# Performance work log

Measured on AMD Instinct MI355X. Metric: run time of the kernel, lower is better.

Reference implementation:

```python
import jax, jax.numpy as jnp
import numpy as np

HEADS = 16
LN_EPS = 1e-6

def _layernorm(x, scale, bias):
    mu = jnp.mean(x, axis=-1, keepdims=True)
    var = jnp.mean(jnp.square(x - mu), axis=-1, keepdims=True)
    return (x - mu) * jax.lax.rsqrt(var + LN_EPS) * scale + bias

def setup_inputs() -> dict:
    key = jax.random.key(0)
    ks = jax.random.split(key, 5)
    B, L, D, F = 2, 2048, 1024, 4096
    s = lambda fan_in: 1.0 / np.sqrt(fan_in)
    return {
        'x': jax.random.normal(ks[0], (B, L, D), jnp.float32),
        'ln1_scale': jnp.ones((D,), jnp.float32),
        'ln1_bias': jnp.zeros((D,), jnp.float32),
        'w_qkv': jax.random.normal(ks[1], (D, 3 * D), jnp.float32) * s(D),
        'w_proj': jax.random.normal(ks[2], (D, D), jnp.float32) * s(D),
        'b_proj': jnp.zeros((D,), jnp.float32),
        'ln2_scale': jnp.ones((D,), jnp.float32),
        'ln2_bias': jnp.zeros((D,), jnp.float32),
        'w_mlp1': jax.random.normal(ks[3], (D, F), jnp.float32) * s(D),
        'b_mlp1': jnp.zeros((F,), jnp.float32),
        'w_mlp2': jax.random.normal(ks[4], (F, D), jnp.float32) * s(F),
        'b_mlp2': jnp.zeros((D,), jnp.float32),
    }

def reference(x, ln1_scale, ln1_bias, w_qkv, w_proj, b_proj,
              ln2_scale, ln2_bias, w_mlp1, b_mlp1, w_mlp2, b_mlp2):
    B, L, D = x.shape
    H = HEADS
    hd = D // H
    # pre-norm attention
    h = _layernorm(x, ln1_scale, ln1_bias)
    qkv = h @ w_qkv  # [B,L,3D]
    q, k, v = jnp.split(qkv, 3, axis=-1)
    q = q.reshape(B, L, H, hd).transpose(0, 2, 1, 3)  # [B,H,L,hd]
    k = k.reshape(B, L, H, hd).transpose(0, 2, 1, 3)
    v = v.reshape(B, L, H, hd).transpose(0, 2, 1, 3)
    scale = jnp.sqrt(jnp.float32(hd))
    scores = jnp.einsum('bhqd,bhkd->bhqk', q, k) / scale  # [B,H,L,L]
    attn = jax.nn.softmax(scores, axis=-1)
    out = jnp.einsum('bhqk,bhkd->bhqd', attn, v)  # [B,H,L,hd]
    out = out.transpose(0, 2, 1, 3).reshape(B, L, D)
    x = x + out @ w_proj + b_proj
    # pre-norm MLP
    h = _layernorm(x, ln2_scale, ln2_bias)
    m = jax.nn.gelu(h @ w_mlp1 + b_mlp1, approximate=True)
    return x + m @ w_mlp2 + b_mlp2
```

## Files before the change

### kernel.cpp

```cpp
#include <hip/hip_runtime.h>
#include <hip/hip_bf16.h>
#include <cstdint>
#include <cstddef>

typedef __bf16 bf16;
typedef __bf16 bf16x8 __attribute__((ext_vector_type(8)));
typedef float f32x4 __attribute__((ext_vector_type(4)));
typedef short short4v __attribute__((ext_vector_type(4)));
typedef unsigned uint2v __attribute__((ext_vector_type(2)));

#define GLB_AS(p) ((const __attribute__((address_space(1))) unsigned*)(unsigned long long)(p))
#define LDS_AS(p) ((__attribute__((address_space(3))) unsigned*)(unsigned)(unsigned long long)(p))

__device__ __forceinline__ void g2l16(const void* g, void* l) {
  __builtin_amdgcn_global_load_lds(GLB_AS(g), LDS_AS(l), 16, 0, 0);
}

__device__ __forceinline__ short f2bf(float x) {
  bf16 h = (bf16)x;
  return __builtin_bit_cast(short, h);
}

__device__ __forceinline__ unsigned pk_bf16(float a, float b) {
  __hip_bfloat162 h = __float22bfloat162_rn(float2{a, b});
  unsigned u;
  __builtin_memcpy(&u, &h, 4);
  return u;
}

extern "C" __device__ __attribute__((const)) float __ocml_native_exp2_f32(float);
extern "C" __device__ __attribute__((const)) float __ocml_native_recip_f32(float);
__device__ __forceinline__ float fast_exp2(float x) {
  return __ocml_native_exp2_f32(x);
}
__device__ __forceinline__ float fast_tanh(float a) {
  float e = __ocml_native_exp2_f32(a * 2.8853900817779268f);
  return 1.f - 2.f * __ocml_native_recip_f32(e + 1.f);
}

constexpr int MROWS = 4096;
constexpr size_t ATILE = (size_t)MROWS * 32;

#define QSCALE 0.18033688011112042f

__device__ __forceinline__ void transpose_body(
    const float* __restrict__ in, bf16* __restrict__ out, int K, int N,
    int bx, int by, float (*tile)[33], int tid)
{
  int tx = tid & 31, ty = tid >> 5;
  int n0 = bx * 32, k0 = by * 32;
  for (int i = ty; i < 32; i += 8)
    tile[i][tx] = in[(size_t)(k0 + i) * N + n0 + tx];
  __syncthreads();
  bf16* obase = out + (size_t)(k0 >> 5) * N * 32;
  for (int i = ty; i < 32; i += 8)
    obase[(size_t)(n0 + i) * 32 + tx] = (bf16)tile[tx][i];
}

__device__ __forceinline__ void ln_body(
    const float* __restrict__ x, const float* __restrict__ sc,
    const float* __restrict__ bi, bf16* __restrict__ out,
    int row, float* wsum, float* wsq, int tid)
{
  const float* xr = x + (size_t)row * 1024;
  int c = tid * 4;
  float4 xv = *(const float4*)(xr + c);
  float s = xv.x + xv.y + xv.z + xv.w;
  float q = xv.x * xv.x + xv.y * xv.y + xv.z * xv.z + xv.w * xv.w;
#pragma unroll
  for (int off = 1; off < 64; off <<= 1) {
    s += __shfl_xor(s, off);
    q += __shfl_xor(q, off);
  }
  int wv = tid >> 6;
  if ((tid & 63) == 0) { wsum[wv] = s; wsq[wv] = q; }
  __syncthreads();
  s = wsum[0] + wsum[1] + wsum[2] + wsum[3];
  q = wsq[0] + wsq[1] + wsq[2] + wsq[3];
  float mean = s * (1.f / 1024.f);
  float var = q * (1.f / 1024.f) - mean * mean;
  float rstd = rsqrtf(var + 1e-6f);
  float4 scv = *(const float4*)(sc + c);
  float4 biv = *(const float4*)(bi + c);
  bf16* o = out + (size_t)(c >> 5) * ATILE + (size_t)row * 32 + (c & 31);
  o[0] = (bf16)((xv.x - mean) * rstd * scv.x + biv.x);
  o[1] = (bf16)((xv.y - mean) * rstd * scv.y + biv.y);
  o[2] = (bf16)((xv.z - mean) * rstd * scv.z + biv.z);
  o[3] = (bf16)((xv.w - mean) * rstd * scv.w + biv.w);
}

__global__ __launch_bounds__(256) void prep_kernel(
    const float* __restrict__ wqkv, const float* __restrict__ wproj,
    const float* __restrict__ wmlp1, const float* __restrict__ wmlp2,
    bf16* __restrict__ wqkv_t, bf16* __restrict__ wproj_t,
    bf16* __restrict__ wmlp1_t, bf16* __restrict__ wmlp2_t,
    const float* __restrict__ x, const float* __restrict__ ln1s,
    const float* __restrict__ ln1b, bf16* __restrict__ hbuf)
{
  __shared__ float tile[32][33];
  __shared__ float wsum[4], wsq[4];
  int bid = blockIdx.x, tid = threadIdx.x;
  if (bid < 3072)
    transpose_body(wqkv, wqkv_t, 1024, 3072, bid % 96, bid / 96, tile, tid);
  else if (bid < 4096) {
    int i = bid - 3072;
    transpose_body(wproj, wproj_t, 1024, 1024, i % 32, i / 32, tile, tid);
  } else if (bid < 8192) {
    int i = bid - 4096;
    transpose_body(wmlp1, wmlp1_t, 1024, 4096, i % 128, i / 128, tile, tid);
  } else if (bid < 12288) {
    int i = bid - 8192;
    transpose_body(wmlp2, wmlp2_t, 4096, 1024, i % 32, i / 32, tile, tid);
  } else {
    ln_body(x, ln1s, ln1b, hbuf, bid - 12288, wsum, wsq, tid);
  }
}

__global__ __launch_bounds__(256) void ln_kernel(
    const float* __restrict__ x, const float* __restrict__ sc,
    const float* __restrict__ bi, bf16* __restrict__ out)
{
  __shared__ float wsum[4], wsq[4];
  ln_body(x, sc, bi, out, blockIdx.x, wsum, wsq, threadIdx.x);
}

template <int MT, int NT, int KS, int EPI>
__global__ __launch_bounds__(256) void gemm_tt(
    const bf16* __restrict__ A, const bf16* __restrict__ Bt,
    int N, int K,
    const float* __restrict__ bias, const float* __restrict__ resid,
    float* __restrict__ outf, bf16* __restrict__ ob0,
    bf16* __restrict__ ob1, bf16* __restrict__ ob2)
{
  constexpr int TM = MT * 32, TN = NT * 32;
  __shared__ __align__(16) bf16 As[2][TM * 32 * KS];
  __shared__ __align__(16) bf16 Bs[2][TN * 32 * KS];
  const int tid = threadIdx.x, lane = tid & 63, wave = tid >> 6;
  const int wm = wave >> 1, wn = wave & 1;
  const int quad = lane >> 4, l16 = lane & 15;

  int flat = blockIdx.x + gridDim.x * blockIdx.y;
  int xcd = flat & 7, rr = flat >> 3;
  int npx = gridDim.x >> 3;
  int bn = xcd * npx + (rr % npx);
  int bm = rr / npx;

  const size_t astride = ATILE;
  const size_t bstride = (size_t)N * 32;
  const bf16* Abase = A + (size_t)bm * TM * 32 + (size_t)lane * 8;
  const bf16* Bbase = Bt + (size_t)bn * TN * 32 + (size_t)lane * 8;

  f32x4 acc[MT][NT] = {};
  const int KT = K / (32 * KS);

  auto stage = [&](int buf, int kt) {
#pragma unroll
    for (int ks = 0; ks < KS; ks++) {
      const bf16* Ab = Abase + (size_t)(kt * KS + ks) * astride;
      const bf16* Bb = Bbase + (size_t)(kt * KS + ks) * bstride;
#pragma unroll
      for (int i = 0; i < MT / 2; i++)
        g2l16(Ab + (wave + 4 * i) * 512, &As[buf][ks * TM * 32 + (wave + 4 * i) * 512]);
#pragma unroll
      for (int i = 0; i < NT / 2; i++)
        g2l16(Bb + (wave + 4 * i) * 512, &Bs[buf][ks * TN * 32 + (wave + 4 * i) * 512]);
    }
  };

  stage(0, 0);
  int buf = 0;
  for (int kt = 0; kt < KT; kt++) {
    __syncthreads();
    if (kt + 1 < KT) stage(buf ^ 1, kt + 1);
#pragma unroll
    for (int kk = 0; kk < KS; kk++) {
      bf16x8 af[MT], bfr[NT];
#pragma unroll
      for (int mt = 0; mt < MT; mt++)
        af[mt] = *(const bf16x8*)&As[buf][kk * TM * 32 + (wm * MT * 16 + mt * 16 + l16) * 32 + quad * 8];
#pragma unroll
      for (int nt = 0; nt < NT; nt++)
        bfr[nt] = *(const bf16x8*)&Bs[buf][kk * TN * 32 + (wn * NT * 16 + nt * 16 + l16) * 32 + quad * 8];
#pragma unroll
      for (int mt = 0; mt < MT; mt++)
#pragma unroll
        for (int nt = 0; nt < NT; nt++)
          acc[mt][nt] = __builtin_amdgcn_mfma_f32_16x16x32_bf16(af[mt], bfr[nt], acc[mt][nt], 0, 0, 0);
    }
    buf ^= 1;
  }

#pragma unroll
  for (int mt = 0; mt < MT; mt++) {
#pragma unroll
    for (int nt = 0; nt < NT; nt++) {
      int row0 = bm * TM + wm * MT * 16 + mt * 16 + quad * 4;
      int col = bn * TN + wn * NT * 16 + nt * 16 + l16;
      if (EPI == 0) {
        int b = row0 >> 11, l = row0 & 2047;
        int which = col >> 10, d = col & 1023;
        int hh = d >> 6, hdi = d & 63;
        size_t bh = (size_t)(b * 16 + hh);
        if (which == 0) {
#pragma unroll
          for (int r = 0; r < 4; r++)
            ob0[(bh * 2048 + l + r) * 64 + hdi] = (bf16)(acc[mt][nt][r] * QSCALE);
        } else if (which == 1) {
#pragma unroll
          for (int r = 0; r < 4; r++)
            ob1[(bh * 2048 + l + r) * 64 + hdi] = (bf16)acc[mt][nt][r];
        } else {
          short4v v4;
#pragma unroll
          for (int r = 0; r < 4; r++) v4[r] = f2bf(acc[mt][nt][r]);
          *(short4v*)&ob2[(bh * 64 + hdi) * 2048 + l] = v4;
        }
      } else {
#pragma unroll
        for (int r = 0; r < 4; r++) {
          int row = row0 + r;
          float v = acc[mt][nt][r];
          if (EPI == 1) {
            size_t idx = (size_t)row * N + col;
            outf[idx] = v + bias[col] + resid[idx];
          } else {
            float t = v + bias[col];
            float a = 0.7978845608028654f * t * (1.f + 0.044715f * t * t);
            float g = 0.5f * t * (1.f + fast_tanh(a));
            ob0[(size_t)(col >> 5) * ATILE + (size_t)row * 32 + (col & 31)] = (bf16)g;
          }
        }
      }
    }
  }
}

__global__ __launch_bounds__(256, 2) void flash_attn(
    const bf16* __restrict__ Q, const bf16* __restrict__ Kg,
    const bf16* __restrict__ Vg, bf16* __restrict__ O)
{
  __shared__ __align__(16) bf16 Ks[128 * 72];
  __shared__ __align__(16) bf16 Vs[64 * 136];
  const int tid = threadIdx.x, lane = tid & 63, wave = tid >> 6;
  const int quad = lane >> 4, l16 = lane & 15;
  const int qt = blockIdx.x, bh = blockIdx.y;
  const int b = bh >> 4, h = bh & 15;

  const bf16* qg = Q + ((size_t)bh * 2048 + qt * 128) * 64;
  const bf16* kg = Kg + (size_t)bh * 2048 * 64;
  const bf16* vg = Vg + (size_t)bh * 64 * 2048;

  bf16x8 qf[2][2];
#pragma unroll
  for (int s = 0; s < 2; s++)
#pragma unroll
    for (int kk = 0; kk < 2; kk++)
      qf[s][kk] = *(const bf16x8*)&qg[(size_t)(wave * 32 + s * 16 + l16) * 64 + kk * 32 + quad * 8];

  f32x4 oacc[2][4] = {};
  float lrow[2] = {0.f, 0.f};

  bf16x8 kreg[4], vreg[4];
#pragma unroll
  for (int i = 0; i < 4; i++) {
    int t = tid + i * 256;
    kreg[i] = *(const bf16x8*)&kg[(size_t)(t >> 3) * 64 + (t & 7) * 8];
    vreg[i] = *(const bf16x8*)&vg[(size_t)(t >> 4) * 2048 + (t & 15) * 8];
  }

  for (int kt = 0; kt < 16; kt++) {
    __syncthreads();
#pragma unroll
    for (int i = 0; i < 4; i++) {
      int t = tid + i * 256;
      *(bf16x8*)&Ks[(t >> 3) * 72 + (t & 7) * 8] = kreg[i];
      *(bf16x8*)&Vs[(t >> 4) * 136 + (t & 15) * 8] = vreg[i];
    }
    __syncthreads();
    if (kt < 15) {
#pragma unroll
      for (int i = 0; i < 4; i++) {
        int t = tid + i * 256;
        kreg[i] = *(const bf16x8*)&kg[((size_t)(kt + 1) * 128 + (t >> 3)) * 64 + (t & 7) * 8];
        vreg[i] = *(const bf16x8*)&vg[(size_t)(t >> 4) * 2048 + (kt + 1) * 128 + (t & 15) * 8];
      }
    }

    f32x4 sacc[2][8] = {};
#pragma unroll
    for (int kk = 0; kk < 2; kk++) {
#pragma unroll
      for (int ct = 0; ct < 8; ct++) {
        bf16x8 kf = *(const bf16x8*)&Ks[(ct * 16 + l16) * 72 + kk * 32 + quad * 8];
        sacc[0][ct] = __builtin_amdgcn_mfma_f32_16x16x32_bf16(kf, qf[0][kk], sacc[0][ct], 0, 0, 0);
        sacc[1][ct] = __builtin_amdgcn_mfma_f32_16x16x32_bf16(kf, qf[1][kk], sacc[1][ct], 0, 0, 0);
      }
    }

    short4v pf[2][8];
#pragma unroll
    for (int s = 0; s < 2; s++) {
      float sum = 0.f;
#pragma unroll
      for (int ct = 0; ct < 8; ct++) {
        float p0 = fast_exp2(sacc[s][ct][0]);
        float p1 = fast_exp2(sacc[s][ct][1]);
        float p2 = fast_exp2(sacc[s][ct][2]);
        float p3 = fast_exp2(sacc[s][ct][3]);
        sum += (p0 + p1) + (p2 + p3);
        uint2v u;
        u[0] = pk_bf16(p0, p1);
        u[1] = pk_bf16(p2, p3);
        pf[s][ct] = __builtin_bit_cast(short4v, u);
      }
      lrow[s] += sum;
    }

#pragma unroll
    for (int ot = 0; ot < 4; ot++) {
#pragma unroll
      for (int ct = 0; ct < 8; ct++) {
        short4v vf = *(const short4v*)&Vs[(ot * 16 + l16) * 136 + ct * 16 + quad * 4];
        oacc[0][ot] = __builtin_amdgcn_mfma_f32_16x16x16bf16_1k(vf, pf[0][ct], oacc[0][ot], 0, 0, 0);
        oacc[1][ot] = __builtin_amdgcn_mfma_f32_16x16x16bf16_1k(vf, pf[1][ct], oacc[1][ot], 0, 0, 0);
      }
    }
  }

#pragma unroll
  for (int s = 0; s < 2; s++) {
    float l = lrow[s];
    l += __shfl_xor(l, 16);
    l += __shfl_xor(l, 32);
    float inv = 1.f / l;
    int qrow = qt * 128 + wave * 32 + s * 16 + l16;
    size_t grow = (size_t)b * 2048 + qrow;
#pragma unroll
    for (int ot = 0; ot < 4; ot++) {
      int col = h * 64 + ot * 16 + quad * 4;
      short4v o4;
#pragma unroll
      for (int r = 0; r < 4; r++) o4[r] = f2bf(oacc[s][ot][r] * inv);
      *(short4v*)&O[(size_t)(col >> 5) * ATILE + grow * 32 + (col & 31)] = o4;
    }
  }
}

extern "C" void kernel_launch(void* const* d_in, const int* in_sizes, int n_in,
                              void* d_out, int out_size, void* d_ws, size_t ws_size,
                              hipStream_t stream)
{
  const float* x     = (const float*)d_in[0];
  const float* ln1s  = (const float*)d_in[1];
  const float* ln1b  = (const float*)d_in[2];
  const float* wqkv  = (const float*)d_in[3];
  const float* wproj = (const float*)d_in[4];
  const float* bproj = (const float*)d_in[5];
  const float* ln2s  = (const float*)d_in[6];
  const float* ln2b  = (const float*)d_in[7];
  const float* wmlp1 = (const float*)d_in[8];
  const float* bmlp1 = (const float*)d_in[9];
  const float* wmlp2 = (const float*)d_in[10];
  const float* bmlp2 = (const float*)d_in[11];
  float* out = (float*)d_out;

  char* ws = (char*)d_ws;
  bf16* wqkv_t  = (bf16*)(ws + 0);
  bf16* wproj_t = (bf16*)(ws + 6291456);
  bf16* wmlp1_t = (bf16*)(ws + 8388608);
  bf16* wmlp2_t = (bf16*)(ws + 16777216);
  bf16* hbuf    = (bf16*)(ws + 25165824);
  bf16* qb      = (bf16*)(ws + 33554432);
  bf16* kb      = (bf16*)(ws + 41943040);
  bf16* vb      = (bf16*)(ws + 50331648);
  bf16* aout    = (bf16*)(ws + 58720256);
  bf16* mbuf    = (bf16*)(ws + 33554432);

  prep_kernel<<<16384, 256, 0, stream>>>(wqkv, wproj, wmlp1, wmlp2,
                                         wqkv_t, wproj_t, wmlp1_t, wmlp2_t,
                                         x, ln1s, ln1b, hbuf);
  gemm_tt<4, 4, 1, 0><<<dim3(24, 32), 256, 0, stream>>>(hbuf, wqkv_t, 3072, 1024,
                                                        nullptr, nullptr, nullptr, qb, kb, vb);
  flash_attn<<<dim3(16, 32), 256, 0, stream>>>(qb, kb, vb, aout);
  gemm_tt<2, 4, 2, 1><<<dim3(8, 64), 256, 0, stream>>>(aout, wproj_t, 1024, 1024,
                                                       bproj, x, out, nullptr, nullptr, nullptr);
  ln_kernel<<<4096, 256, 0, stream>>>(out, ln2s, ln2b, hbuf);
  gemm_tt<4, 4, 1, 2><<<dim3(32, 32), 256, 0, stream>>>(hbuf, wmlp1_t, 4096, 1024,
                                                        bmlp1, nullptr, nullptr, mbuf, nullptr, nullptr);
  gemm_tt<2, 4, 2, 1><<<dim3(8, 64), 256, 0, stream>>>(mbuf, wmlp2_t, 1024, 4096,
                                                       bmlp2, out, out, nullptr, nullptr, nullptr);
}
```

Baseline: 313.3 us.

## Use 8 waves per attention block with XOR-swizzled LDS and MFMA priority

The flash attention kernel goes from 4 waves each handling 32 query rows to 8 waves each handling 16 rows. This halves per-thread register state and raises the occupancy target. The padded K/V LDS tiles are replaced by unpadded tiles with an XOR swizzle to avoid bank conflicts. s_setprio is raised around the MFMA phases so waves can overlap matrix work with softmax. Each K fragment read from LDS is now reused for only one query subtile instead of two, so LDS read traffic per MFMA increases.

```diff
diff --git a/kernel.cpp b/kernel.cpp
--- a/kernel.cpp
+++ b/kernel.cpp
@@ -235,12 +235,12 @@
   }
 }
 
-__global__ __launch_bounds__(256, 2) void flash_attn(
+__global__ __launch_bounds__(512, 4) void flash_attn(
     const bf16* __restrict__ Q, const bf16* __restrict__ Kg,
     const bf16* __restrict__ Vg, bf16* __restrict__ O)
 {
-  __shared__ __align__(16) bf16 Ks[128 * 72];
-  __shared__ __align__(16) bf16 Vs[64 * 136];
+  __shared__ __align__(16) bf16 Ks[128 * 64];
+  __shared__ __align__(16) bf16 Vs[64 * 128];
   const int tid = threadIdx.x, lane = tid & 63, wave = tid >> 6;
   const int quad = lane >> 4, l16 = lane & 15;
   const int qt = blockIdx.x, bh = blockIdx.y;
@@ -250,20 +250,21 @@
   const bf16* kg = Kg + (size_t)bh * 2048 * 64;
   const bf16* vg = Vg + (size_t)bh * 64 * 2048;
 
-  bf16x8 qf[2][2];
-#pragma unroll
-  for (int s = 0; s < 2; s++)
-#pragma unroll
-    for (int kk = 0; kk < 2; kk++)
-      qf[s][kk] = *(const bf16x8*)&qg[(size_t)(wave * 32 + s * 16 + l16) * 64 + kk * 32 + quad * 8];
-
-  f32x4 oacc[2][4] = {};
-  float lrow[2] = {0.f, 0.f};
-
-  bf16x8 kreg[4], vreg[4];
-#pragma unroll
-  for (int i = 0; i < 4; i++) {
-    int t = tid + i * 256;
+  const int kw0 = ((tid >> 3) << 7) + (((tid & 7) << 4) ^ (((tid >> 3) & 7) << 4));
+  const int vw0 = ((tid >> 4) << 8) + (((tid & 15) << 4) ^ (((tid >> 4) & 7) << 4));
+
+  bf16x8 qf[2];
+#pragma unroll
+  for (int kk = 0; kk < 2; kk++)
+    qf[kk] = *(const bf16x8*)&qg[(size_t)(wave * 16 + l16) * 64 + kk * 32 + quad * 8];
+
+  f32x4 oacc[4] = {};
+  float lrow = 0.f;
+
+  bf16x8 kreg[2], vreg[2];
+#pragma unroll
+  for (int i = 0; i < 2; i++) {
+    int t = tid + i * 512;
     kreg[i] = *(const bf16x8*)&kg[(size_t)(t >> 3) * 64 + (t & 7) * 8];
     vreg[i] = *(const bf16x8*)&vg[(size_t)(t >> 4) * 2048 + (t & 15) * 8];
   }
@@ -271,76 +272,79 @@
   for (int kt = 0; kt < 16; kt++) {
     __syncthreads();
 #pragma unroll
-    for (int i = 0; i < 4; i++) {
-      int t = tid + i * 256;
-      *(bf16x8*)&Ks[(t >> 3) * 72 + (t & 7) * 8] = kreg[i];
-      *(bf16x8*)&Vs[(t >> 4) * 136 + (t & 15) * 8] = vreg[i];
+    for (int i = 0; i < 2; i++) {
+      *(bf16x8*)((char*)Ks + kw0 + i * 64 * 128) = kreg[i];
+      *(bf16x8*)((char*)Vs + vw0 + i * 32 * 256) = vreg[i];
     }
     __syncthreads();
     if (kt < 15) {
 #pragma unroll
-      for (int i = 0; i < 4; i++) {
-        int t = tid + i * 256;
+      for (int i = 0; i < 2; i++) {
+        int t = tid + i * 512;
         kreg[i] = *(const bf16x8*)&kg[((size_t)(kt + 1) * 128 + (t >> 3)) * 64 + (t & 7) * 8];
         vreg[i] = *(const bf16x8*)&vg[(size_t)(t >> 4) * 2048 + (kt + 1) * 128 + (t & 15) * 8];
       }
     }
 
-    f32x4 sacc[2][8] = {};
+    f32x4 sacc[8] = {};
+    __builtin_amdgcn_s_setprio(1);
 #pragma unroll
     for (int kk = 0; kk < 2; kk++) {
 #pragma unroll
       for (int ct = 0; ct < 8; ct++) {
-        bf16x8 kf = *(const bf16x8*)&Ks[(ct * 16 + l16) * 72 + kk * 32 + quad * 8];
-        sacc[0][ct] = __builtin_amdgcn_mfma_f32_16x16x32_bf16(kf, qf[0][kk], sacc[0][ct], 0, 0, 0);
-        sacc[1][ct] = __builtin_amdgcn_mfma_f32_16x16x32_bf16(kf, qf[1][kk], sacc[1][ct], 0, 0, 0);
-      }
-    }
-
-    short4v pf[2][8];
-#pragma unroll
-    for (int s = 0; s < 2; s++) {
+        int krow = ct * 16 + l16;
+        int kcol = (kk * 64 + quad * 16) ^ ((krow & 7) << 4);
+        bf16x8 kf = *(const bf16x8*)((const char*)Ks + krow * 128 + kcol);
+        sacc[ct] = __builtin_amdgcn_mfma_f32_16x16x32_bf16(kf, qf[kk], sacc[ct], 0, 0, 0);
+      }
+    }
+    __builtin_amdgcn_s_setprio(0);
+
+    short4v pf[8];
+    {
       float sum = 0.f;
 #pragma unroll
       for (int ct = 0; ct < 8; ct++) {
-        float p0 = fast_exp2(sacc[s][ct][0]);
-        float p1 = fast_exp2(sacc[s][ct][1]);
-        float p2 = fast_exp2(sacc[s][ct][2]);
-        float p3 = fast_exp2(sacc[s][ct][3]);
+        float p0 = fast_exp2(sacc[ct][0]);
+        float p1 = fast_exp2(sacc[ct][1]);
+        float p2 = fast_exp2(sacc[ct][2]);
+        float p3 = fast_exp2(sacc[ct][3]);
         sum += (p0 + p1) + (p2 + p3);
         uint2v u;
         u[0] = pk_bf16(p0, p1);
         u[1] = pk_bf16(p2, p3);
-        pf[s][ct] = __builtin_bit_cast(short4v, u);
-      }
-      lrow[s] += sum;
-    }
-
+        pf[ct] = __builtin_bit_cast(short4v, u);
+      }
+      lrow += sum;
+    }
+
+    __builtin_amdgcn_s_setprio(1);
 #pragma unroll
     for (int ot = 0; ot < 4; ot++) {
 #pragma unroll
       for (int ct = 0; ct < 8; ct++) {
-        short4v vf = *(const short4v*)&Vs[(ot * 16 + l16) * 136 + ct * 16 + quad * 4];
-        oacc[0][ot] = __builtin_amdgcn_mfma_f32_16x16x16bf16_1k(vf, pf[0][ct], oacc[0][ot], 0, 0, 0);
-        oacc[1][ot] = __builtin_amdgcn_mfma_f32_16x16x16bf16_1k(vf, pf[1][ct], oacc[1][ot], 0, 0, 0);
-      }
-    }
-  }
-
-#pragma unroll
-  for (int s = 0; s < 2; s++) {
-    float l = lrow[s];
+        int vrow = ot * 16 + l16;
+        int vcol = (ct * 32 + quad * 8) ^ ((vrow & 7) << 4);
+        short4v vf = *(const short4v*)((const char*)Vs + vrow * 256 + vcol);
+        oacc[ot] = __builtin_amdgcn_mfma_f32_16x16x16bf16_1k(vf, pf[ct], oacc[ot], 0, 0, 0);
+      }
+    }
+    __builtin_amdgcn_s_setprio(0);
+  }
+
+  {
+    float l = lrow;
     l += __shfl_xor(l, 16);
     l += __shfl_xor(l, 32);
     float inv = 1.f / l;
-    int qrow = qt * 128 + wave * 32 + s * 16 + l16;
+    int qrow = qt * 128 + wave * 16 + l16;
     size_t grow = (size_t)b * 2048 + qrow;
 #pragma unroll
     for (int ot = 0; ot < 4; ot++) {
       int col = h * 64 + ot * 16 + quad * 4;
       short4v o4;
 #pragma unroll
-      for (int r = 0; r < 4; r++) o4[r] = f2bf(oacc[s][ot][r] * inv);
+      for (int r = 0; r < 4; r++) o4[r] = f2bf(oacc[ot][r] * inv);
       *(short4v*)&O[(size_t)(col >> 5) * ATILE + grow * 32 + (col & 31)] = o4;
     }
   }
@@ -381,7 +385,7 @@
                                          x, ln1s, ln1b, hbuf);
   gemm_tt<4, 4, 1, 0><<<dim3(24, 32), 256, 0, stream>>>(hbuf, wqkv_t, 3072, 1024,
                                                         nullptr, nullptr, nullptr, qb, kb, vb);
-  flash_attn<<<dim3(16, 32), 256, 0, stream>>>(qb, kb, vb, aout);
+  flash_attn<<<dim3(16, 32), 512, 0, stream>>>(qb, kb, vb, aout);
   gemm_tt<2, 4, 2, 1><<<dim3(8, 64), 256, 0, stream>>>(aout, wproj_t, 1024, 1024,
                                                        bproj, x, out, nullptr, nullptr, nullptr);
   ln_kernel<<<4096, 256, 0, stream>>>(out, ln2s, ln2b, hbuf);
```

Result: slower. 341.4 us (+9.0%).
